# Kernel optimization log

Measured on AMD Instinct MI355X. Metric: run time of the kernel, lower is better.

## Reference

```python
import jax, jax.numpy as jnp
import numpy as np

# Model dims (hardcoded by the hw-accurate numerics: >>6 mean -> d_model=64, 45/256 ~ 1/sqrt(32) -> head_dim=32)
D_MODEL = 64; N_HEADS = 2; HEAD_DIM = 32; D_FF = 256
N_LAYERS = 4; VOCAB = 8192; CTX = 1024; B = 4; T = 1024


def _ste(x, y):
    # forward value y, straight-through gradient of x
    return x + jax.lax.stop_gradient(y - x)


def ste_round_clamp(x, lo, hi):
    return _ste(x, jnp.clip(jnp.round(x), lo, hi))


def ste_round_clamp_int8(x):
    return ste_round_clamp(x, -128.0, 127.0)


def ste_shift_right(x, n):
    s = x * (0.5 ** n)
    return _ste(s, jnp.floor(s))


def ste_hw_int8(x):
    # hardware truncation to signed 8 bits (wrap-around, not clamp)
    return _ste(x, jnp.mod(x + 128.0, 256.0) - 128.0)


def bitlinear_hw(x, w):
    # ternary weights via STE (BitNet b1.58 style), int accumulate, >>6 requant, int8 clamp
    scale = jnp.maximum(jnp.mean(jnp.abs(w)), 1e-5)
    w_t = ste_round_clamp(w / scale, -1.0, 1.0)
    acc = jnp.einsum('btc,oc->bto', x, w_t)
    return ste_round_clamp_int8(ste_shift_right(acc, 6))


def rmsnorm_hw(x, weight):
    x_int = ste_round_clamp_int8(x)
    sum_sq = jnp.sum(x_int * x_int, axis=-1, keepdims=True)
    mean_sq = ste_shift_right(sum_sq, 6)                       # /64 == /d_model
    lut_idx = jnp.clip(ste_shift_right(mean_sq, 6), 0.0, 255.0)
    bin_center = jnp.maximum(lut_idx * 64.0 + 32.0, 1.0)
    inv_rms = ste_round_clamp(16384.0 / jnp.sqrt(bin_center), 0.0, 16383.0)
    w_c = weight + jax.lax.stop_gradient(jnp.clip(weight, -2.0, 2.0) - weight)
    gamma_q = ste_round_clamp(w_c * 1024.0, -32768.0, 32767.0)  # Q5.10
    p1 = ste_shift_right(x_int * inv_rms, 8)
    y = ste_shift_right(p1 * gamma_q, 10)
    return ste_round_clamp_int8(y)


def hw_softmax(scores):
    # 4-segment piecewise-linear exp + uint8 normalization (Softmax.scala)
    m = jnp.max(scores, axis=-1, keepdims=True)
    sh = scores - m
    ea = jnp.where(sh >= -3.0, 256.0 + sh * 64.0,
         jnp.where(sh >= -8.0, 64.0 + (sh + 3.0) * 11.0,
         jnp.where(sh >= -24.0, sh + 24.0, 0.0)))
    s = jnp.maximum(jnp.sum(ea, axis=-1, keepdims=True), 1.0)
    return ste_round_clamp(ea / s * 255.0, 0.0, 255.0)


def _forward(tokens, tok_emb, pos_emb, attn_norm_w, q_w, k_w, v_w, o_w,
             ff_norm_w, up_w, down_w, final_norm_w):
    positions = jnp.arange(T)
    tok_q = ste_round_clamp(tok_emb[tokens] * 1024.0, -32768.0, 32767.0)
    pos_q = ste_round_clamp(pos_emb[positions] * 1024.0, -32768.0, 32767.0)
    x = ste_hw_int8(ste_shift_right(tok_q + pos_q[None], 3))   # [B,T,D]
    causal = jnp.triu(jnp.ones((T, T), dtype=bool), k=1)
    for i in range(N_LAYERS):
        # attention block
        h = rmsnorm_hw(x, attn_norm_w[i])
        q = bitlinear_hw(h, q_w[i]).reshape(B, T, N_HEADS, HEAD_DIM).transpose(0, 2, 1, 3)
        k = bitlinear_hw(h, k_w[i]).reshape(B, T, N_HEADS, HEAD_DIM).transpose(0, 2, 1, 3)
        v = bitlinear_hw(h, v_w[i]).reshape(B, T, N_HEADS, HEAD_DIM).transpose(0, 2, 1, 3)
        scores = ste_shift_right(jnp.einsum('bhqd,bhkd->bhqk', q, k) * 45.0, 8)
        scores = jnp.where(causal, -32767.0, scores)
        probs = hw_softmax(scores)                              # uint8-valued
        a = ste_hw_int8(ste_shift_right(jnp.einsum('bhqk,bhkd->bhqd', probs, v), 8))
        a = a.transpose(0, 2, 1, 3).reshape(B, T, D_MODEL)
        a = bitlinear_hw(a, o_w[i])
        x = ste_hw_int8(x + a)
        # FFN block
        h = rmsnorm_hw(x, ff_norm_w[i])
        u = ste_round_clamp_int8(jax.nn.relu(bitlinear_hw(h, up_w[i])))
        x = ste_hw_int8(x + bitlinear_hw(u, down_w[i]))
    x = rmsnorm_hw(x, final_norm_w)
    # hw logits: INT8 activations x Q5.10 tied embedding, dequant + 1/sqrt(d) scale
    emb_q = ste_round_clamp(tok_emb * 1024.0, -32768.0, 32767.0)
    logits = jnp.einsum('btd,vd->btv', x, emb_q) * (D_MODEL ** -0.5 / 1024.0)
    return logits


def setup_inputs() -> dict:
    key = jax.random.key(0)
    ks = jax.random.split(key, 12)
    std = 0.02
    inp = {
        'tokens': jax.random.randint(ks[0], (B, T), 0, VOCAB),
        'tok_emb': jax.random.normal(ks[1], (VOCAB, D_MODEL), jnp.float32),  # default N(0,1)
        'pos_emb': std * jax.random.normal(ks[2], (CTX, D_MODEL), jnp.float32),
        'attn_norm_w': jnp.ones((N_LAYERS, D_MODEL), jnp.float32),
        'q_w': std * jax.random.normal(ks[3], (N_LAYERS, D_MODEL, D_MODEL), jnp.float32),
        'k_w': std * jax.random.normal(ks[4], (N_LAYERS, D_MODEL, D_MODEL), jnp.float32),
        'v_w': std * jax.random.normal(ks[5], (N_LAYERS, D_MODEL, D_MODEL), jnp.float32),
        'o_w': std * jax.random.normal(ks[6], (N_LAYERS, D_MODEL, D_MODEL), jnp.float32),
        'ff_norm_w': jnp.ones((N_LAYERS, D_MODEL), jnp.float32),
        'up_w': std * jax.random.normal(ks[7], (N_LAYERS, D_FF, D_MODEL), jnp.float32),
        'down_w': std * jax.random.normal(ks[8], (N_LAYERS, D_MODEL, D_FF), jnp.float32),
        'final_norm_w': jnp.ones((D_MODEL,), jnp.float32),
    }
    return inp


def reference(tokens, tok_emb, pos_emb, attn_norm_w, q_w, k_w, v_w, o_w,
              ff_norm_w, up_w, down_w, final_norm_w):
    return _forward(tokens, tok_emb, pos_emb, attn_norm_w, q_w, k_w, v_w, o_w,
                    ff_norm_w, up_w, down_w, final_norm_w)
```

## Files before the change

### kernel.cpp

```cpp
#include <hip/hip_runtime.h>
#include <stdint.h>

#define T_CTX 1024
#define DM 64
#define NH 2
#define HD 32
#define DFF 256
#define NVOCAB 8192

typedef int v4i __attribute__((ext_vector_type(4)));

__device__ __forceinline__ int clampi(int v, int lo, int hi){ return v<lo?lo:(v>hi?hi:v); }
__device__ __forceinline__ int wrap8(int v){ return ((v + 128) & 255) - 128; }
__device__ __forceinline__ int sdot4(int a, int b, int c){ return __builtin_amdgcn_sdot4(a, b, c, false); }

__device__ __forceinline__ int wave_reduce_add(int v){
  #pragma unroll
  for (int off = 1; off < 64; off <<= 1) v += __shfl_xor(v, off, 64);
  return v;
}
__device__ __forceinline__ int wave_reduce_max(int v){
  #pragma unroll
  for (int off = 1; off < 64; off <<= 1){ int o = __shfl_xor(v, off, 64); v = o > v ? o : v; }
  return v;
}

__device__ __forceinline__ int rmsnorm_one(int xv, int g){
  int ss  = wave_reduce_add(xv * xv);
  int ms  = ss >> 6;
  int lut = ms >> 6; if (lut > 255) lut = 255;
  int bc  = lut * 64 + 32;
  int inv = (int)__builtin_rint(16384.0 / __builtin_sqrt((double)bc));
  int p1  = (xv * inv) >> 8;
  int y   = (p1 * g) >> 10;
  return clampi(y, -128, 127);
}

__global__ __launch_bounds__(256) void prep_weights(
    const float* __restrict__ qw, const float* __restrict__ kw, const float* __restrict__ vw,
    const float* __restrict__ ow, const float* __restrict__ uw, const float* __restrict__ dw,
    const float* __restrict__ anw, const float* __restrict__ fnw, const float* __restrict__ finw,
    int8_t* __restrict__ wt, int16_t* __restrict__ gq)
{
  int tid = threadIdx.x;
  int bid = blockIdx.x;
  if (bid < 24) {
    int layer = bid / 6, kind = bid % 6;
    const float* src; int n; int off;
    switch (kind) {
      case 0:  src = qw + layer*4096;  n = 4096;  off = 0;     break;
      case 1:  src = kw + layer*4096;  n = 4096;  off = 4096;  break;
      case 2:  src = vw + layer*4096;  n = 4096;  off = 8192;  break;
      case 3:  src = ow + layer*4096;  n = 4096;  off = 12288; break;
      case 4:  src = uw + layer*16384; n = 16384; off = 16384; break;
      default: src = dw + layer*16384; n = 16384; off = 32768; break;
    }
    __shared__ double sred[256];
    double s = 0.0;
    for (int i = tid; i < n; i += 256) s += (double)__builtin_fabsf(src[i]);
    sred[tid] = s; __syncthreads();
    for (int st = 128; st > 0; st >>= 1){ if (tid < st) sred[tid] += sred[tid + st]; __syncthreads(); }
    float fs = (float)(sred[0] / (double)n);
    if (fs < 1e-5f) fs = 1e-5f;
    int8_t* dst = wt + layer*49152 + off;
    for (int i = tid; i < n; i += 256) {
      int t = (int)__builtin_rintf(src[i] / fs);
      dst[i] = (int8_t)clampi(t, -1, 1);
    }
  } else {
    for (int i = tid; i < 576; i += 256) {
      int norm = i >> 6, c = i & 63;
      const float* wsrc = (norm < 4) ? (anw + norm*64) : (norm < 8) ? (fnw + (norm-4)*64) : finw;
      float wv = wsrc[c];
      float wc = wv < -2.0f ? -2.0f : (wv > 2.0f ? 2.0f : wv);
      gq[i] = (int16_t)clampi((int)__builtin_rintf(wc * 1024.0f), -32768, 32767);
    }
  }
}

__global__ __launch_bounds__(256) void prep_emb_kernel(
    const float* __restrict__ tok_emb, int8_t* __restrict__ elo, int8_t* __restrict__ ehi)
{
  int i = blockIdx.x * 256 + threadIdx.x;
  if (i < NVOCAB * DM) {
    int e  = clampi((int)__builtin_rintf(tok_emb[i] * 1024.0f), -32768, 32767);
    int l  = ((e + 128) & 255) - 128;
    int hh = (e - l) >> 8;
    if (hh > 127) hh = 127;
    elo[i] = (int8_t)l; ehi[i] = (int8_t)hh;
  }
}

__global__ __launch_bounds__(256) void token_stage(
    const int* __restrict__ tokens, const float* __restrict__ tok_emb, const float* __restrict__ pos_emb,
    int8_t* __restrict__ x, const int8_t* __restrict__ aArr,
    int8_t* __restrict__ qA, int8_t* __restrict__ kA, int8_t* __restrict__ vT,
    const int8_t* __restrict__ wt, const int16_t* __restrict__ gq, int8_t* __restrict__ xf,
    int do_embed, int post_layer, int pre_layer, int do_final)
{
  __shared__ int8_t sh8[4][DFF];
  int w = threadIdx.x >> 6, lane = threadIdx.x & 63;
  int t = blockIdx.x * 4 + w;
  int8_t* myS = sh8[w];
  int xv;
  if (do_embed) {
    int tok = tokens[t];
    int s = t & (T_CTX - 1);
    int tq = clampi((int)__builtin_rintf(tok_emb[tok*DM + lane] * 1024.0f), -32768, 32767);
    int pq = clampi((int)__builtin_rintf(pos_emb[s*DM + lane] * 1024.0f), -32768, 32767);
    xv = wrap8((tq + pq) >> 3);
  } else {
    xv = (int)x[t*DM + lane];
  }
  if (post_layer >= 0) {
    const int8_t* wtL = wt + post_layer*49152;
    myS[lane] = aArr[t*DM + lane];
    __syncthreads();
    {
      const int* a4 = (const int*)myS;
      const int* wo = (const int*)(wtL + 12288);
      int acc = 0;
      #pragma unroll
      for (int i = 0; i < 16; i++) acc = sdot4(a4[i], wo[lane*16 + i], acc);
      xv = wrap8(xv + clampi(acc >> 6, -128, 127));
    }
    __syncthreads();
    int h2 = rmsnorm_one(xv, (int)gq[(4 + post_layer)*DM + lane]);
    myS[lane] = (int8_t)h2;
    __syncthreads();
    int uv[4];
    {
      const int* h4 = (const int*)myS;
      const int* wu = (const int*)(wtL + 16384);
      #pragma unroll
      for (int jj = 0; jj < 4; jj++) {
        int j = jj*64 + lane;
        int acc = 0;
        #pragma unroll
        for (int i = 0; i < 16; i++) acc = sdot4(h4[i], wu[j*16 + i], acc);
        int u = clampi(acc >> 6, -128, 127);
        uv[jj] = u < 0 ? 0 : u;
      }
    }
    __syncthreads();
    #pragma unroll
    for (int jj = 0; jj < 4; jj++) myS[jj*64 + lane] = (int8_t)uv[jj];
    __syncthreads();
    {
      const int* u4 = (const int*)myS;
      const int* wd = (const int*)(wtL + 32768);
      int acc = 0;
      #pragma unroll
      for (int i = 0; i < 64; i++) acc = sdot4(u4[i], wd[lane*64 + i], acc);
      xv = wrap8(xv + clampi(acc >> 6, -128, 127));
    }
    __syncthreads();
  }
  x[t*DM + lane] = (int8_t)xv;
  if (pre_layer >= 0) {
    int h = rmsnorm_one(xv, (int)gq[pre_layer*DM + lane]);
    myS[lane] = (int8_t)h;
    __syncthreads();
    const int8_t* wtL = wt + pre_layer*49152;
    const int* h4 = (const int*)myS;
    int b = t >> 10, s = t & (T_CTX - 1);
    int hh = lane >> 5, d = lane & 31;
    int bhh = b*NH + hh;
    {
      const int* wm = (const int*)(wtL + 0);
      int acc = 0;
      #pragma unroll
      for (int i = 0; i < 16; i++) acc = sdot4(h4[i], wm[lane*16 + i], acc);
      qA[(bhh*T_CTX + s)*HD + d] = (int8_t)clampi(acc >> 6, -128, 127);
    }
    {
      const int* wm = (const int*)(wtL + 4096);
      int acc = 0;
      #pragma unroll
      for (int i = 0; i < 16; i++) acc = sdot4(h4[i], wm[lane*16 + i], acc);
      kA[(bhh*T_CTX + s)*HD + d] = (int8_t)clampi(acc >> 6, -128, 127);
    }
    {
      const int* wm = (const int*)(wtL + 8192);
      int acc = 0;
      #pragma unroll
      for (int i = 0; i < 16; i++) acc = sdot4(h4[i], wm[lane*16 + i], acc);
      vT[(bhh*HD + d)*T_CTX + s] = (int8_t)clampi(acc >> 6, -128, 127);
    }
  }
  if (do_final) {
    int h = rmsnorm_one(xv, (int)gq[8*DM + lane]);
    xf[t*DM + lane] = (int8_t)h;
  }
}

__global__ __launch_bounds__(256) void attn_kernel(
    const int8_t* __restrict__ qA, const int8_t* __restrict__ kA, const int8_t* __restrict__ vT,
    int8_t* __restrict__ aOut)
{
  __shared__ int vt32[32*257];
  __shared__ int sp32[4][256];
  int w = threadIdx.x >> 6, lane = threadIdx.x & 63;
  int bh = blockIdx.x & 7, qblk = blockIdx.x >> 3;
  int qi = 1023 - 4*qblk - w;
  int b = bh >> 1, h = bh & 1;
  const int8_t* qBase = qA + bh*(T_CTX*HD);
  const int8_t* kBase = kA + bh*(T_CTX*HD);
  const int8_t* vTbh  = vT + bh*(HD*T_CTX);

  #pragma unroll
  for (int r = 0; r < 8; r++) {
    int d = r*4 + w;
    int4 v = *(const int4*)(vTbh + d*T_CTX + lane*16);
    int* dst = vt32 + d*257 + lane*4;
    dst[0] = v.x; dst[1] = v.y; dst[2] = v.z; dst[3] = v.w;
  }

  const int4* qr = (const int4*)(qBase + qi*HD);
  int4 qa = qr[0], qb = qr[1];
  int sc[16];
  int mloc = -(1 << 30);
  #pragma unroll
  for (int j = 0; j < 16; j++) {
    int k = lane + j*64;
    int s;
    if (k <= qi) {
      const int4* kr = (const int4*)(kBase + k*HD);
      int4 ka = kr[0], kb = kr[1];
      int d = 0;
      d = sdot4(qa.x, ka.x, d); d = sdot4(qa.y, ka.y, d);
      d = sdot4(qa.z, ka.z, d); d = sdot4(qa.w, ka.w, d);
      d = sdot4(qb.x, kb.x, d); d = sdot4(qb.y, kb.y, d);
      d = sdot4(qb.z, kb.z, d); d = sdot4(qb.w, kb.w, d);
      s = (d * 45) >> 8;
    } else s = -(1 << 30);
    sc[j] = s; if (s > mloc) mloc = s;
  }
  int m = wave_reduce_max(mloc);
  int ssum = 0;
  #pragma unroll
  for (int j = 0; j < 16; j++) {
    int k = lane + j*64;
    int e = 0;
    if (k <= qi) {
      int sh = sc[j] - m;
      e = (sh >= -3) ? (256 + sh*64)
        : (sh >= -8) ? (64 + (sh + 3)*11)
        : (sh >= -24) ? (sh + 24) : 0;
    }
    sc[j] = e; ssum += e;
  }
  int s0 = wave_reduce_add(ssum); if (s0 < 1) s0 = 1;
  float sf = (float)s0;
  uint8_t* spb = (uint8_t*)sp32[w];
  #pragma unroll
  for (int j = 0; j < 16; j++) {
    int k = lane + j*64;
    int p = (int)__builtin_rintf((float)sc[j] / sf * 255.0f);
    spb[k] = (uint8_t)clampi(p, 0, 255);
  }
  __syncthreads();

  int dg = lane & 7, kc = lane >> 3;
  const int* vr0 = vt32 + (dg*4 + 0)*257;
  const int* vr1 = vt32 + (dg*4 + 1)*257;
  const int* vr2 = vt32 + (dg*4 + 2)*257;
  const int* vr3 = vt32 + (dg*4 + 3)*257;
  const int* spw = sp32[w];
  int hi0=0, hi1=0, hi2=0, hi3=0, lo0=0, lo1=0, lo2=0, lo3=0;
  int cmax = qi >> 2;
  for (int c = kc; c <= cmax; c += 8) {
    int p4 = spw[c];
    int ph = (p4 >> 1) & 0x7f7f7f7f;
    int pl = p4 & 0x01010101;
    int v0 = vr0[c], v1 = vr1[c], v2 = vr2[c], v3 = vr3[c];
    hi0 = sdot4(ph, v0, hi0); lo0 = sdot4(pl, v0, lo0);
    hi1 = sdot4(ph, v1, hi1); lo1 = sdot4(pl, v1, lo1);
    hi2 = sdot4(ph, v2, hi2); lo2 = sdot4(pl, v2, lo2);
    hi3 = sdot4(ph, v3, hi3); lo3 = sdot4(pl, v3, lo3);
  }
  int a0 = 2*hi0 + lo0, a1 = 2*hi1 + lo1, a2 = 2*hi2 + lo2, a3 = 2*hi3 + lo3;
  #pragma unroll
  for (int off = 8; off < 64; off <<= 1) {
    a0 += __shfl_xor(a0, off, 64);
    a1 += __shfl_xor(a1, off, 64);
    a2 += __shfl_xor(a2, off, 64);
    a3 += __shfl_xor(a3, off, 64);
  }
  if (kc == 0) {
    int r0 = wrap8(a0 >> 8) & 255;
    int r1 = wrap8(a1 >> 8) & 255;
    int r2 = wrap8(a2 >> 8) & 255;
    int r3 = wrap8(a3 >> 8) & 255;
    int packed = r0 | (r1 << 8) | (r2 << 16) | (r3 << 24);
    *(int*)(aOut + (b*T_CTX + qi)*DM + h*HD + dg*4) = packed;
  }
}

__global__ __launch_bounds__(256) void logits_kernel(
    const int8_t* __restrict__ xf, const int8_t* __restrict__ elo, const int8_t* __restrict__ ehi,
    float* __restrict__ out)
{
  int w = threadIdx.x >> 6, lane = threadIdx.x & 63;
  int m = lane & 15, quad = lane >> 4;
  int tokBase = blockIdx.y * 64 + w * 16;
  v4i A = *(const v4i*)(xf + (tokBase + m)*DM + quad*16);
  #pragma unroll
  for (int tile = 0; tile < 8; tile++) {
    int vocBase = blockIdx.x * 128 + tile * 16;
    v4i Blo = *(const v4i*)(elo + (vocBase + m)*DM + quad*16);
    v4i Bhi = *(const v4i*)(ehi + (vocBase + m)*DM + quad*16);
    v4i zero = {0, 0, 0, 0};
    v4i dLo = __builtin_amdgcn_mfma_i32_16x16x64_i8(A, Blo, zero, 0, 0, 0);
    v4i dHi = __builtin_amdgcn_mfma_i32_16x16x64_i8(A, Bhi, zero, 0, 0, 0);
    #pragma unroll
    for (int r = 0; r < 4; r++) {
      int val = dLo[r] + (dHi[r] << 8);
      int row = tokBase + quad*4 + r;
      int col = vocBase + m;
      out[row*NVOCAB + col] = (float)val * 1.220703125e-4f;
    }
  }
}

extern "C" void kernel_launch(void* const* d_in, const int* in_sizes, int n_in,
                              void* d_out, int out_size, void* d_ws, size_t ws_size,
                              hipStream_t stream)
{
  const int*   tokens  = (const int*)d_in[0];
  const float* tok_emb = (const float*)d_in[1];
  const float* pos_emb = (const float*)d_in[2];
  const float* attn_nw = (const float*)d_in[3];
  const float* q_w     = (const float*)d_in[4];
  const float* k_w     = (const float*)d_in[5];
  const float* v_w     = (const float*)d_in[6];
  const float* o_w     = (const float*)d_in[7];
  const float* ff_nw   = (const float*)d_in[8];
  const float* up_w    = (const float*)d_in[9];
  const float* dn_w    = (const float*)d_in[10];
  const float* fin_nw  = (const float*)d_in[11];
  float* out = (float*)d_out;
  char* ws = (char*)d_ws;

  int8_t*  x   = (int8_t*)(ws + 0);
  int8_t*  a   = (int8_t*)(ws + 262144);
  int8_t*  qA  = (int8_t*)(ws + 524288);
  int8_t*  kA  = (int8_t*)(ws + 786432);
  int8_t*  vT  = (int8_t*)(ws + 1048576);
  int8_t*  wt  = (int8_t*)(ws + 1310720);
  int8_t*  elo = (int8_t*)(ws + 1507328);
  int8_t*  ehi = (int8_t*)(ws + 2031616);
  int16_t* gq  = (int16_t*)(ws + 2555904);
  int8_t*  xf  = (int8_t*)(ws + 2560000);

  prep_weights<<<25, 256, 0, stream>>>(q_w, k_w, v_w, o_w, up_w, dn_w, attn_nw, ff_nw, fin_nw, wt, gq);
  prep_emb_kernel<<<2048, 256, 0, stream>>>(tok_emb, elo, ehi);
  token_stage<<<1024, 256, 0, stream>>>(tokens, tok_emb, pos_emb, x, a, qA, kA, vT, wt, gq, xf,
                                        1, -1, 0, 0);
  for (int L = 0; L < 4; L++) {
    attn_kernel<<<2048, 256, 0, stream>>>(qA, kA, vT, a);
    int pre = (L < 3) ? (L + 1) : -1;
    int fin = (L == 3) ? 1 : 0;
    token_stage<<<1024, 256, 0, stream>>>(tokens, tok_emb, pos_emb, x, a, qA, kA, vT, wt, gq, xf,
                                          0, L, pre, fin);
  }
  logits_kernel<<<dim3(64, 64), 256, 0, stream>>>(xf, elo, ehi, out);
}
```

Baseline: 359.8 us.

## Fuse all stages into one persistent cooperative kernel with grid syncs

Replaces the eleven separate kernel launches (weight prep, embedding prep, token stages, attention, logits) with a single cooperative persistent kernel that loops over virtual blocks and uses grid.sync between phases. Attention work is paired (vb and 2047-vb) so causal-length imbalance is evened out per block. This removes launch overhead and inter-kernel gaps, at the cost of grid-wide barriers, a fixed occupancy-limited grid, and shared-memory aliasing across phases.

Result: slower. 923.0 us (+156.5%).

```diff
diff --git a/kernel.cpp b/kernel.cpp
--- a/kernel.cpp
+++ b/kernel.cpp
@@ -1,5 +1,8 @@
 #include <hip/hip_runtime.h>
+#include <hip/hip_cooperative_groups.h>
 #include <stdint.h>
+
+namespace cg = cooperative_groups;
 
 #define T_CTX 1024
 #define DM 64
@@ -36,72 +39,18 @@
   return clampi(y, -128, 127);
 }
 
-__global__ __launch_bounds__(256) void prep_weights(
-    const float* __restrict__ qw, const float* __restrict__ kw, const float* __restrict__ vw,
-    const float* __restrict__ ow, const float* __restrict__ uw, const float* __restrict__ dw,
-    const float* __restrict__ anw, const float* __restrict__ fnw, const float* __restrict__ finw,
-    int8_t* __restrict__ wt, int16_t* __restrict__ gq)
-{
-  int tid = threadIdx.x;
-  int bid = blockIdx.x;
-  if (bid < 24) {
-    int layer = bid / 6, kind = bid % 6;
-    const float* src; int n; int off;
-    switch (kind) {
-      case 0:  src = qw + layer*4096;  n = 4096;  off = 0;     break;
-      case 1:  src = kw + layer*4096;  n = 4096;  off = 4096;  break;
-      case 2:  src = vw + layer*4096;  n = 4096;  off = 8192;  break;
-      case 3:  src = ow + layer*4096;  n = 4096;  off = 12288; break;
-      case 4:  src = uw + layer*16384; n = 16384; off = 16384; break;
-      default: src = dw + layer*16384; n = 16384; off = 32768; break;
-    }
-    __shared__ double sred[256];
-    double s = 0.0;
-    for (int i = tid; i < n; i += 256) s += (double)__builtin_fabsf(src[i]);
-    sred[tid] = s; __syncthreads();
-    for (int st = 128; st > 0; st >>= 1){ if (tid < st) sred[tid] += sred[tid + st]; __syncthreads(); }
-    float fs = (float)(sred[0] / (double)n);
-    if (fs < 1e-5f) fs = 1e-5f;
-    int8_t* dst = wt + layer*49152 + off;
-    for (int i = tid; i < n; i += 256) {
-      int t = (int)__builtin_rintf(src[i] / fs);
-      dst[i] = (int8_t)clampi(t, -1, 1);
-    }
-  } else {
-    for (int i = tid; i < 576; i += 256) {
-      int norm = i >> 6, c = i & 63;
-      const float* wsrc = (norm < 4) ? (anw + norm*64) : (norm < 8) ? (fnw + (norm-4)*64) : finw;
-      float wv = wsrc[c];
-      float wc = wv < -2.0f ? -2.0f : (wv > 2.0f ? 2.0f : wv);
-      gq[i] = (int16_t)clampi((int)__builtin_rintf(wc * 1024.0f), -32768, 32767);
-    }
-  }
-}
-
-__global__ __launch_bounds__(256) void prep_emb_kernel(
-    const float* __restrict__ tok_emb, int8_t* __restrict__ elo, int8_t* __restrict__ ehi)
-{
-  int i = blockIdx.x * 256 + threadIdx.x;
-  if (i < NVOCAB * DM) {
-    int e  = clampi((int)__builtin_rintf(tok_emb[i] * 1024.0f), -32768, 32767);
-    int l  = ((e + 128) & 255) - 128;
-    int hh = (e - l) >> 8;
-    if (hh > 127) hh = 127;
-    elo[i] = (int8_t)l; ehi[i] = (int8_t)hh;
-  }
-}
-
-__global__ __launch_bounds__(256) void token_stage(
-    const int* __restrict__ tokens, const float* __restrict__ tok_emb, const float* __restrict__ pos_emb,
-    int8_t* __restrict__ x, const int8_t* __restrict__ aArr,
+__device__ __forceinline__ void token_phase(
+    int blk, const int* __restrict__ tokens, const float* __restrict__ tok_emb,
+    const float* __restrict__ pos_emb, int8_t* __restrict__ x, const int8_t* __restrict__ aArr,
     int8_t* __restrict__ qA, int8_t* __restrict__ kA, int8_t* __restrict__ vT,
     const int8_t* __restrict__ wt, const int16_t* __restrict__ gq, int8_t* __restrict__ xf,
-    int do_embed, int post_layer, int pre_layer, int do_final)
+    int do_embed, int post_layer, int pre_layer, int do_final,
+    int8_t (*sh8)[DFF])
 {
-  __shared__ int8_t sh8[4][DFF];
   int w = threadIdx.x >> 6, lane = threadIdx.x & 63;
-  int t = blockIdx.x * 4 + w;
+  int t = blk * 4 + w;
   int8_t* myS = sh8[w];
+  __syncthreads();
   int xv;
   if (do_embed) {
     int tok = tokens[t];
@@ -194,19 +143,20 @@
   }
 }
 
-__global__ __launch_bounds__(256) void attn_kernel(
-    const int8_t* __restrict__ qA, const int8_t* __restrict__ kA, const int8_t* __restrict__ vT,
-    int8_t* __restrict__ aOut)
+__device__ __forceinline__ void attn_phase(
+    int vb, const int8_t* __restrict__ qA, const int8_t* __restrict__ kA,
+    const int8_t* __restrict__ vT, int8_t* __restrict__ aOut,
+    int* vt32, int (*sp32)[256])
 {
-  __shared__ int vt32[32*257];
-  __shared__ int sp32[4][256];
   int w = threadIdx.x >> 6, lane = threadIdx.x & 63;
-  int bh = blockIdx.x & 7, qblk = blockIdx.x >> 3;
+  int bh = vb & 7, qblk = vb >> 3;
   int qi = 1023 - 4*qblk - w;
   int b = bh >> 1, h = bh & 1;
   const int8_t* qBase = qA + bh*(T_CTX*HD);
   const int8_t* kBase = kA + bh*(T_CTX*HD);
   const int8_t* vTbh  = vT + bh*(HD*T_CTX);
+
+  __syncthreads();
 
   #pragma unroll
   for (int r = 0; r < 8; r++) {
@@ -297,28 +247,114 @@
   }
 }
 
-__global__ __launch_bounds__(256) void logits_kernel(
-    const int8_t* __restrict__ xf, const int8_t* __restrict__ elo, const int8_t* __restrict__ ehi,
-    float* __restrict__ out)
+__global__ __launch_bounds__(256, 4) void fused(
+    const int* __restrict__ tokens, const float* __restrict__ tok_emb, const float* __restrict__ pos_emb,
+    const float* __restrict__ anw, const float* __restrict__ qw, const float* __restrict__ kw,
+    const float* __restrict__ vw, const float* __restrict__ ow, const float* __restrict__ fnw,
+    const float* __restrict__ uw, const float* __restrict__ dw, const float* __restrict__ finw,
+    float* __restrict__ out, char* __restrict__ ws)
 {
-  int w = threadIdx.x >> 6, lane = threadIdx.x & 63;
-  int m = lane & 15, quad = lane >> 4;
-  int tokBase = blockIdx.y * 64 + w * 16;
-  v4i A = *(const v4i*)(xf + (tokBase + m)*DM + quad*16);
-  #pragma unroll
-  for (int tile = 0; tile < 8; tile++) {
-    int vocBase = blockIdx.x * 128 + tile * 16;
-    v4i Blo = *(const v4i*)(elo + (vocBase + m)*DM + quad*16);
-    v4i Bhi = *(const v4i*)(ehi + (vocBase + m)*DM + quad*16);
-    v4i zero = {0, 0, 0, 0};
-    v4i dLo = __builtin_amdgcn_mfma_i32_16x16x64_i8(A, Blo, zero, 0, 0, 0);
-    v4i dHi = __builtin_amdgcn_mfma_i32_16x16x64_i8(A, Bhi, zero, 0, 0, 0);
+  __shared__ __align__(16) int smem[32*257 + 4*256];
+  int* vt32 = smem;
+  int (*sp32)[256] = (int(*)[256])(smem + 32*257);
+  int8_t (*sh8)[DFF] = (int8_t(*)[DFF])smem;
+  double* sred = (double*)smem;
+
+  int8_t*  x   = (int8_t*)(ws + 0);
+  int8_t*  a   = (int8_t*)(ws + 262144);
+  int8_t*  qA  = (int8_t*)(ws + 524288);
+  int8_t*  kA  = (int8_t*)(ws + 786432);
+  int8_t*  vT  = (int8_t*)(ws + 1048576);
+  int8_t*  wt  = (int8_t*)(ws + 1310720);
+  int8_t*  elo = (int8_t*)(ws + 1507328);
+  int8_t*  ehi = (int8_t*)(ws + 2031616);
+  int16_t* gq  = (int16_t*)(ws + 2555904);
+  int8_t*  xf  = (int8_t*)(ws + 2560000);
+
+  cg::grid_group grid = cg::this_grid();
+  int tid = threadIdx.x, bid = blockIdx.x, nb = gridDim.x;
+
+  if (bid < 24) {
+    int layer = bid / 6, kind = bid % 6;
+    const float* src; int n; int off;
+    switch (kind) {
+      case 0:  src = qw + layer*4096;  n = 4096;  off = 0;     break;
+      case 1:  src = kw + layer*4096;  n = 4096;  off = 4096;  break;
+      case 2:  src = vw + layer*4096;  n = 4096;  off = 8192;  break;
+      case 3:  src = ow + layer*4096;  n = 4096;  off = 12288; break;
+      case 4:  src = uw + layer*16384; n = 16384; off = 16384; break;
+      default: src = dw + layer*16384; n = 16384; off = 32768; break;
+    }
+    double s = 0.0;
+    for (int i = tid; i < n; i += 256) s += (double)__builtin_fabsf(src[i]);
+    sred[tid] = s; __syncthreads();
+    for (int st = 128; st > 0; st >>= 1){ if (tid < st) sred[tid] += sred[tid + st]; __syncthreads(); }
+    float fs = (float)(sred[0] / (double)n);
+    if (fs < 1e-5f) fs = 1e-5f;
+    int8_t* dst = wt + layer*49152 + off;
+    for (int i = tid; i < n; i += 256) {
+      int t = (int)__builtin_rintf(src[i] / fs);
+      dst[i] = (int8_t)clampi(t, -1, 1);
+    }
+  } else if (bid == 24) {
+    for (int i = tid; i < 576; i += 256) {
+      int norm = i >> 6, c = i & 63;
+      const float* wsrc = (norm < 4) ? (anw + norm*64) : (norm < 8) ? (fnw + (norm-4)*64) : finw;
+      float wv = wsrc[c];
+      float wc = wv < -2.0f ? -2.0f : (wv > 2.0f ? 2.0f : wv);
+      gq[i] = (int16_t)clampi((int)__builtin_rintf(wc * 1024.0f), -32768, 32767);
+    }
+  } else {
+    int base = (bid - 25)*256 + tid;
+    int stride = (nb - 25)*256;
+    for (int i = base; i < NVOCAB*DM; i += stride) {
+      int e  = clampi((int)__builtin_rintf(tok_emb[i] * 1024.0f), -32768, 32767);
+      int l  = ((e + 128) & 255) - 128;
+      int hh = (e - l) >> 8;
+      if (hh > 127) hh = 127;
+      elo[i] = (int8_t)l; ehi[i] = (int8_t)hh;
+    }
+  }
+  grid.sync();
+
+  for (int vb = bid; vb < 1024; vb += nb)
+    token_phase(vb, tokens, tok_emb, pos_emb, x, a, qA, kA, vT, wt, gq, xf, 1, -1, 0, 0, sh8);
+  grid.sync();
+
+  for (int L = 0; L < 4; L++) {
+    for (int vb = bid; vb < 1024; vb += nb) {
+      attn_phase(vb,        qA, kA, vT, a, vt32, sp32);
+      attn_phase(2047 - vb, qA, kA, vT, a, vt32, sp32);
+    }
+    grid.sync();
+    int pre = (L < 3) ? (L + 1) : -1;
+    int fin = (L == 3) ? 1 : 0;
+    for (int vb = bid; vb < 1024; vb += nb)
+      token_phase(vb, tokens, tok_emb, pos_emb, x, a, qA, kA, vT, wt, gq, xf, 0, L, pre, fin, sh8);
+    grid.sync();
+  }
+
+  for (int vb = bid; vb < 4096; vb += nb) {
+    int by = vb >> 6, bx = vb & 63;
+    int w = tid >> 6, lane = tid & 63;
+    int m = lane & 15, quad = lane >> 4;
+    int tokBase = by * 64 + w * 16;
+    v4i A = *(const v4i*)(xf + (tokBase + m)*DM + quad*16);
     #pragma unroll
-    for (int r = 0; r < 4; r++) {
-      int val = dLo[r] + (dHi[r] << 8);
-      int row = tokBase + quad*4 + r;
-      int col = vocBase + m;
-      out[row*NVOCAB + col] = (float)val * 1.220703125e-4f;
+    for (int tile = 0; tile < 8; tile++) {
+      int vocBase = bx * 128 + tile * 16;
+      v4i Blo = *(const v4i*)(elo + (vocBase + m)*DM + quad*16);
+      v4i Bhi = *(const v4i*)(ehi + (vocBase + m)*DM + quad*16);
+      v4i zero = {0, 0, 0, 0};
+      v4i dLo = __builtin_amdgcn_mfma_i32_16x16x64_i8(A, Blo, zero, 0, 0, 0);
+      v4i dHi = __builtin_amdgcn_mfma_i32_16x16x64_i8(A, Bhi, zero, 0, 0, 0);
+      #pragma unroll
+      for (int r = 0; r < 4; r++) {
+        int val = dLo[r] + (dHi[r] << 8);
+        int row = tokBase + quad*4 + r;
+        int col = vocBase + m;
+        out[row*NVOCAB + col] = (float)val * 1.220703125e-4f;
+      }
     }
   }
 }
@@ -342,27 +378,22 @@
   float* out = (float*)d_out;
   char* ws = (char*)d_ws;
 
-  int8_t*  x   = (int8_t*)(ws + 0);
-  int8_t*  a   = (int8_t*)(ws + 262144);
-  int8_t*  qA  = (int8_t*)(ws + 524288);
-  int8_t*  kA  = (int8_t*)(ws + 786432);
-  int8_t*  vT  = (int8_t*)(ws + 1048576);
-  int8_t*  wt  = (int8_t*)(ws + 1310720);
-  int8_t*  elo = (int8_t*)(ws + 1507328);
-  int8_t*  ehi = (int8_t*)(ws + 2031616);
-  int16_t* gq  = (int16_t*)(ws + 2555904);
-  int8_t*  xf  = (int8_t*)(ws + 2560000);
-
-  prep_weights<<<25, 256, 0, stream>>>(q_w, k_w, v_w, o_w, up_w, dn_w, attn_nw, ff_nw, fin_nw, wt, gq);
-  prep_emb_kernel<<<2048, 256, 0, stream>>>(tok_emb, elo, ehi);
-  token_stage<<<1024, 256, 0, stream>>>(tokens, tok_emb, pos_emb, x, a, qA, kA, vT, wt, gq, xf,
-                                        1, -1, 0, 0);
-  for (int L = 0; L < 4; L++) {
-    attn_kernel<<<2048, 256, 0, stream>>>(qA, kA, vT, a);
-    int pre = (L < 3) ? (L + 1) : -1;
-    int fin = (L == 3) ? 1 : 0;
-    token_stage<<<1024, 256, 0, stream>>>(tokens, tok_emb, pos_emb, x, a, qA, kA, vT, wt, gq, xf,
-                                          0, L, pre, fin);
-  }
-  logits_kernel<<<dim3(64, 64), 256, 0, stream>>>(xf, elo, ehi, out);
-}
+  static int nblk = 0;
+  if (nblk == 0) {
+    int perCU = 0;
+    if (hipOccupancyMaxActiveBlocksPerMultiprocessor(&perCU, (const void*)fused, 256, 0) != hipSuccess
+        || perCU < 1) perCU = 4;
+    int dev = 0; hipGetDevice(&dev);
+    hipDeviceProp_t prop{};
+    int ncu = 256;
+    if (hipGetDeviceProperties(&prop, dev) == hipSuccess && prop.multiProcessorCount > 0)
+      ncu = prop.multiProcessorCount;
+    long tot = (long)perCU * (long)ncu;
+    nblk = (int)(tot < 1024 ? tot : 1024);
+    if (nblk < 26) nblk = 26;
+  }
+
+  void* args[] = { &tokens, &tok_emb, &pos_emb, &attn_nw, &q_w, &k_w, &v_w, &o_w,
+                   &ff_nw, &up_w, &dn_w, &fin_nw, &out, &ws };
+  hipLaunchCooperativeKernel((const void*)fused, dim3(nblk), dim3(256), args, 0, stream);
+}
```

## Fuse attention with per-token MLP stage and merge prep kernels

Applied to the files above, without the earlier changes.

Attention for two queries times two heads per block is now fused with the output projection, FFN, next-layer norm and QKV projection, so the attention output never goes through global memory. Q/K/V are double-buffered across layers so the fused kernel can write the next layer's inputs while other blocks still read the current ones. The two prep kernels become one launch, and V is read straight from global memory instead of being staged in shared memory. In exchange, half the waves sit idle during the MLP phase, the 2048-block grid means each block handles fewer tokens, and the uncached V reads may cost bandwidth.

New measurement: 429.7 us. 19.4% more time.

```diff
diff --git a/kernel.cpp b/kernel.cpp
--- a/kernel.cpp
+++ b/kernel.cpp
@@ -36,11 +36,13 @@
   return clampi(y, -128, 127);
 }
 
-__global__ __launch_bounds__(256) void prep_weights(
+__global__ __launch_bounds__(256) void prep_all(
     const float* __restrict__ qw, const float* __restrict__ kw, const float* __restrict__ vw,
     const float* __restrict__ ow, const float* __restrict__ uw, const float* __restrict__ dw,
     const float* __restrict__ anw, const float* __restrict__ fnw, const float* __restrict__ finw,
-    int8_t* __restrict__ wt, int16_t* __restrict__ gq)
+    const float* __restrict__ tok_emb,
+    int8_t* __restrict__ wt, int16_t* __restrict__ gq,
+    int8_t* __restrict__ elo, int8_t* __restrict__ ehi)
 {
   int tid = threadIdx.x;
   int bid = blockIdx.x;
@@ -67,7 +69,7 @@
       int t = (int)__builtin_rintf(src[i] / fs);
       dst[i] = (int8_t)clampi(t, -1, 1);
     }
-  } else {
+  } else if (bid == 24) {
     for (int i = tid; i < 576; i += 256) {
       int norm = i >> 6, c = i & 63;
       const float* wsrc = (norm < 4) ? (anw + norm*64) : (norm < 8) ? (fnw + (norm-4)*64) : finw;
@@ -75,146 +77,84 @@
       float wc = wv < -2.0f ? -2.0f : (wv > 2.0f ? 2.0f : wv);
       gq[i] = (int16_t)clampi((int)__builtin_rintf(wc * 1024.0f), -32768, 32767);
     }
-  }
-}
-
-__global__ __launch_bounds__(256) void prep_emb_kernel(
-    const float* __restrict__ tok_emb, int8_t* __restrict__ elo, int8_t* __restrict__ ehi)
-{
-  int i = blockIdx.x * 256 + threadIdx.x;
-  if (i < NVOCAB * DM) {
-    int e  = clampi((int)__builtin_rintf(tok_emb[i] * 1024.0f), -32768, 32767);
-    int l  = ((e + 128) & 255) - 128;
-    int hh = (e - l) >> 8;
-    if (hh > 127) hh = 127;
-    elo[i] = (int8_t)l; ehi[i] = (int8_t)hh;
-  }
-}
-
-__global__ __launch_bounds__(256) void token_stage(
+  } else {
+    int i = (bid - 25)*256 + tid;
+    if (i < NVOCAB * DM) {
+      int e  = clampi((int)__builtin_rintf(tok_emb[i] * 1024.0f), -32768, 32767);
+      int l  = ((e + 128) & 255) - 128;
+      int hh = (e - l) >> 8;
+      if (hh > 127) hh = 127;
+      elo[i] = (int8_t)l; ehi[i] = (int8_t)hh;
+    }
+  }
+}
+
+__global__ __launch_bounds__(256) void embed_pre0(
     const int* __restrict__ tokens, const float* __restrict__ tok_emb, const float* __restrict__ pos_emb,
-    int8_t* __restrict__ x, const int8_t* __restrict__ aArr,
-    int8_t* __restrict__ qA, int8_t* __restrict__ kA, int8_t* __restrict__ vT,
-    const int8_t* __restrict__ wt, const int16_t* __restrict__ gq, int8_t* __restrict__ xf,
-    int do_embed, int post_layer, int pre_layer, int do_final)
-{
-  __shared__ int8_t sh8[4][DFF];
+    int8_t* __restrict__ x, int8_t* __restrict__ qA, int8_t* __restrict__ kA, int8_t* __restrict__ vT,
+    const int8_t* __restrict__ wt, const int16_t* __restrict__ gq)
+{
+  __shared__ int8_t sh8[4][64];
   int w = threadIdx.x >> 6, lane = threadIdx.x & 63;
   int t = blockIdx.x * 4 + w;
-  int8_t* myS = sh8[w];
-  int xv;
-  if (do_embed) {
-    int tok = tokens[t];
-    int s = t & (T_CTX - 1);
-    int tq = clampi((int)__builtin_rintf(tok_emb[tok*DM + lane] * 1024.0f), -32768, 32767);
-    int pq = clampi((int)__builtin_rintf(pos_emb[s*DM + lane] * 1024.0f), -32768, 32767);
-    xv = wrap8((tq + pq) >> 3);
-  } else {
-    xv = (int)x[t*DM + lane];
-  }
-  if (post_layer >= 0) {
-    const int8_t* wtL = wt + post_layer*49152;
-    myS[lane] = aArr[t*DM + lane];
-    __syncthreads();
-    {
-      const int* a4 = (const int*)myS;
-      const int* wo = (const int*)(wtL + 12288);
-      int acc = 0;
-      #pragma unroll
-      for (int i = 0; i < 16; i++) acc = sdot4(a4[i], wo[lane*16 + i], acc);
-      xv = wrap8(xv + clampi(acc >> 6, -128, 127));
-    }
-    __syncthreads();
-    int h2 = rmsnorm_one(xv, (int)gq[(4 + post_layer)*DM + lane]);
-    myS[lane] = (int8_t)h2;
-    __syncthreads();
-    int uv[4];
-    {
-      const int* h4 = (const int*)myS;
-      const int* wu = (const int*)(wtL + 16384);
-      #pragma unroll
-      for (int jj = 0; jj < 4; jj++) {
-        int j = jj*64 + lane;
-        int acc = 0;
-        #pragma unroll
-        for (int i = 0; i < 16; i++) acc = sdot4(h4[i], wu[j*16 + i], acc);
-        int u = clampi(acc >> 6, -128, 127);
-        uv[jj] = u < 0 ? 0 : u;
-      }
-    }
-    __syncthreads();
-    #pragma unroll
-    for (int jj = 0; jj < 4; jj++) myS[jj*64 + lane] = (int8_t)uv[jj];
-    __syncthreads();
-    {
-      const int* u4 = (const int*)myS;
-      const int* wd = (const int*)(wtL + 32768);
-      int acc = 0;
-      #pragma unroll
-      for (int i = 0; i < 64; i++) acc = sdot4(u4[i], wd[lane*64 + i], acc);
-      xv = wrap8(xv + clampi(acc >> 6, -128, 127));
-    }
-    __syncthreads();
-  }
+  int tok = tokens[t];
+  int s = t & (T_CTX - 1);
+  int tq = clampi((int)__builtin_rintf(tok_emb[tok*DM + lane] * 1024.0f), -32768, 32767);
+  int pq = clampi((int)__builtin_rintf(pos_emb[s*DM + lane] * 1024.0f), -32768, 32767);
+  int xv = wrap8((tq + pq) >> 3);
   x[t*DM + lane] = (int8_t)xv;
-  if (pre_layer >= 0) {
-    int h = rmsnorm_one(xv, (int)gq[pre_layer*DM + lane]);
-    myS[lane] = (int8_t)h;
-    __syncthreads();
-    const int8_t* wtL = wt + pre_layer*49152;
-    const int* h4 = (const int*)myS;
-    int b = t >> 10, s = t & (T_CTX - 1);
-    int hh = lane >> 5, d = lane & 31;
-    int bhh = b*NH + hh;
-    {
-      const int* wm = (const int*)(wtL + 0);
-      int acc = 0;
-      #pragma unroll
-      for (int i = 0; i < 16; i++) acc = sdot4(h4[i], wm[lane*16 + i], acc);
-      qA[(bhh*T_CTX + s)*HD + d] = (int8_t)clampi(acc >> 6, -128, 127);
-    }
-    {
-      const int* wm = (const int*)(wtL + 4096);
-      int acc = 0;
-      #pragma unroll
-      for (int i = 0; i < 16; i++) acc = sdot4(h4[i], wm[lane*16 + i], acc);
-      kA[(bhh*T_CTX + s)*HD + d] = (int8_t)clampi(acc >> 6, -128, 127);
-    }
-    {
-      const int* wm = (const int*)(wtL + 8192);
-      int acc = 0;
-      #pragma unroll
-      for (int i = 0; i < 16; i++) acc = sdot4(h4[i], wm[lane*16 + i], acc);
-      vT[(bhh*HD + d)*T_CTX + s] = (int8_t)clampi(acc >> 6, -128, 127);
-    }
-  }
-  if (do_final) {
-    int h = rmsnorm_one(xv, (int)gq[8*DM + lane]);
-    xf[t*DM + lane] = (int8_t)h;
-  }
-}
-
-__global__ __launch_bounds__(256) void attn_kernel(
+  int h = rmsnorm_one(xv, (int)gq[lane]);
+  sh8[w][lane] = (int8_t)h;
+  __syncthreads();
+  const int* h4 = (const int*)sh8[w];
+  int b = t >> 10;
+  int hh = lane >> 5, d = lane & 31;
+  int bhh = b*NH + hh;
+  const int8_t* wtL = wt;
+  {
+    const int* wm = (const int*)(wtL + 0);
+    int acc = 0;
+    #pragma unroll
+    for (int i = 0; i < 16; i++) acc = sdot4(h4[i], wm[lane*16 + i], acc);
+    qA[(bhh*T_CTX + s)*HD + d] = (int8_t)clampi(acc >> 6, -128, 127);
+  }
+  {
+    const int* wm = (const int*)(wtL + 4096);
+    int acc = 0;
+    #pragma unroll
+    for (int i = 0; i < 16; i++) acc = sdot4(h4[i], wm[lane*16 + i], acc);
+    kA[(bhh*T_CTX + s)*HD + d] = (int8_t)clampi(acc >> 6, -128, 127);
+  }
+  {
+    const int* wm = (const int*)(wtL + 8192);
+    int acc = 0;
+    #pragma unroll
+    for (int i = 0; i < 16; i++) acc = sdot4(h4[i], wm[lane*16 + i], acc);
+    vT[(bhh*HD + d)*T_CTX + s] = (int8_t)clampi(acc >> 6, -128, 127);
+  }
+}
+
+__global__ __launch_bounds__(256) void layer_kernel(
     const int8_t* __restrict__ qA, const int8_t* __restrict__ kA, const int8_t* __restrict__ vT,
-    int8_t* __restrict__ aOut)
-{
-  __shared__ int vt32[32*257];
+    int8_t* __restrict__ x, int8_t* __restrict__ qN, int8_t* __restrict__ kN, int8_t* __restrict__ vN,
+    const int8_t* __restrict__ wt, const int16_t* __restrict__ gq, int8_t* __restrict__ xf,
+    int L, int pre_layer, int do_final)
+{
   __shared__ int sp32[4][256];
+  __shared__ int sh_a32[2][16];
+  __shared__ int8_t sh8[2][256];
+
   int w = threadIdx.x >> 6, lane = threadIdx.x & 63;
-  int bh = blockIdx.x & 7, qblk = blockIdx.x >> 3;
-  int qi = 1023 - 4*qblk - w;
-  int b = bh >> 1, h = bh & 1;
+  int blk = blockIdx.x;
+  int b = blk & 3;
+  int s0 = 1022 - 2*(blk >> 2);
+  int tl = w >> 1;
+  int qi = s0 + tl;
+  int h = w & 1;
+  int bh = b*NH + h;
   const int8_t* qBase = qA + bh*(T_CTX*HD);
   const int8_t* kBase = kA + bh*(T_CTX*HD);
   const int8_t* vTbh  = vT + bh*(HD*T_CTX);
-
-  #pragma unroll
-  for (int r = 0; r < 8; r++) {
-    int d = r*4 + w;
-    int4 v = *(const int4*)(vTbh + d*T_CTX + lane*16);
-    int* dst = vt32 + d*257 + lane*4;
-    dst[0] = v.x; dst[1] = v.y; dst[2] = v.z; dst[3] = v.w;
-  }
 
   const int4* qr = (const int4*)(qBase + qi*HD);
   int4 qa = qr[0], qb = qr[1];
@@ -250,8 +190,8 @@
     }
     sc[j] = e; ssum += e;
   }
-  int s0 = wave_reduce_add(ssum); if (s0 < 1) s0 = 1;
-  float sf = (float)s0;
+  int s0sum = wave_reduce_add(ssum); if (s0sum < 1) s0sum = 1;
+  float sf = (float)s0sum;
   uint8_t* spb = (uint8_t*)sp32[w];
   #pragma unroll
   for (int j = 0; j < 16; j++) {
@@ -262,10 +202,10 @@
   __syncthreads();
 
   int dg = lane & 7, kc = lane >> 3;
-  const int* vr0 = vt32 + (dg*4 + 0)*257;
-  const int* vr1 = vt32 + (dg*4 + 1)*257;
-  const int* vr2 = vt32 + (dg*4 + 2)*257;
-  const int* vr3 = vt32 + (dg*4 + 3)*257;
+  const int* vr0 = (const int*)(vTbh + (dg*4 + 0)*T_CTX);
+  const int* vr1 = (const int*)(vTbh + (dg*4 + 1)*T_CTX);
+  const int* vr2 = (const int*)(vTbh + (dg*4 + 2)*T_CTX);
+  const int* vr3 = (const int*)(vTbh + (dg*4 + 3)*T_CTX);
   const int* spw = sp32[w];
   int hi0=0, hi1=0, hi2=0, hi3=0, lo0=0, lo1=0, lo2=0, lo3=0;
   int cmax = qi >> 2;
@@ -293,7 +233,96 @@
     int r2 = wrap8(a2 >> 8) & 255;
     int r3 = wrap8(a3 >> 8) & 255;
     int packed = r0 | (r1 << 8) | (r2 << 16) | (r3 << 24);
-    *(int*)(aOut + (b*T_CTX + qi)*DM + h*HD + dg*4) = packed;
+    sh_a32[tl][h*8 + dg] = packed;
+  }
+  __syncthreads();
+
+  int t = b*T_CTX + s0 + w;
+  int xv = 0;
+  const int8_t* wtL = wt + L*49152;
+  if (w < 2) {
+    xv = (int)x[t*DM + lane];
+    {
+      const int* a4 = sh_a32[w];
+      const int* wo = (const int*)(wtL + 12288);
+      int acc = 0;
+      #pragma unroll
+      for (int i = 0; i < 16; i++) acc = sdot4(a4[i], wo[lane*16 + i], acc);
+      xv = wrap8(xv + clampi(acc >> 6, -128, 127));
+    }
+    int h2 = rmsnorm_one(xv, (int)gq[(4 + L)*DM + lane]);
+    sh8[w][lane] = (int8_t)h2;
+  }
+  __syncthreads();
+  if (w < 2) {
+    int8_t* myS = sh8[w];
+    const int* h4 = (const int*)myS;
+    int uv[4];
+    {
+      const int* wu = (const int*)(wtL + 16384);
+      #pragma unroll
+      for (int jj = 0; jj < 4; jj++) {
+        int j = jj*64 + lane;
+        int acc = 0;
+        #pragma unroll
+        for (int i = 0; i < 16; i++) acc = sdot4(h4[i], wu[j*16 + i], acc);
+        int u = clampi(acc >> 6, -128, 127);
+        uv[jj] = u < 0 ? 0 : u;
+      }
+    }
+    #pragma unroll
+    for (int jj = 0; jj < 4; jj++) myS[jj*64 + lane] = (int8_t)uv[jj];
+  }
+  __syncthreads();
+  if (w < 2) {
+    const int* u4 = (const int*)sh8[w];
+    {
+      const int* wd = (const int*)(wtL + 32768);
+      int acc = 0;
+      #pragma unroll
+      for (int i = 0; i < 64; i++) acc = sdot4(u4[i], wd[lane*64 + i], acc);
+      xv = wrap8(xv + clampi(acc >> 6, -128, 127));
+    }
+    x[t*DM + lane] = (int8_t)xv;
+  }
+  if (pre_layer >= 0) {
+    if (w < 2) {
+      int hp = rmsnorm_one(xv, (int)gq[pre_layer*DM + lane]);
+      sh8[w][lane] = (int8_t)hp;
+    }
+    __syncthreads();
+    if (w < 2) {
+      const int* h4 = (const int*)sh8[w];
+      const int8_t* wtP = wt + pre_layer*49152;
+      int s = s0 + w;
+      int hh = lane >> 5, d = lane & 31;
+      int bhh = b*NH + hh;
+      {
+        const int* wm = (const int*)(wtP + 0);
+        int acc = 0;
+        #pragma unroll
+        for (int i = 0; i < 16; i++) acc = sdot4(h4[i], wm[lane*16 + i], acc);
+        qN[(bhh*T_CTX + s)*HD + d] = (int8_t)clampi(acc >> 6, -128, 127);
+      }
+      {
+        const int* wm = (const int*)(wtP + 4096);
+        int acc = 0;
+        #pragma unroll
+        for (int i = 0; i < 16; i++) acc = sdot4(h4[i], wm[lane*16 + i], acc);
+        kN[(bhh*T_CTX + s)*HD + d] = (int8_t)clampi(acc >> 6, -128, 127);
+      }
+      {
+        const int* wm = (const int*)(wtP + 8192);
+        int acc = 0;
+        #pragma unroll
+        for (int i = 0; i < 16; i++) acc = sdot4(h4[i], wm[lane*16 + i], acc);
+        vN[(bhh*HD + d)*T_CTX + s] = (int8_t)clampi(acc >> 6, -128, 127);
+      }
+    }
+  }
+  if (do_final && w < 2) {
+    int hf = rmsnorm_one(xv, (int)gq[8*DM + lane]);
+    xf[t*DM + lane] = (int8_t)hf;
   }
 }
 
@@ -342,27 +371,29 @@
   float* out = (float*)d_out;
   char* ws = (char*)d_ws;
 
-  int8_t*  x   = (int8_t*)(ws + 0);
-  int8_t*  a   = (int8_t*)(ws + 262144);
-  int8_t*  qA  = (int8_t*)(ws + 524288);
-  int8_t*  kA  = (int8_t*)(ws + 786432);
-  int8_t*  vT  = (int8_t*)(ws + 1048576);
-  int8_t*  wt  = (int8_t*)(ws + 1310720);
-  int8_t*  elo = (int8_t*)(ws + 1507328);
-  int8_t*  ehi = (int8_t*)(ws + 2031616);
-  int16_t* gq  = (int16_t*)(ws + 2555904);
-  int8_t*  xf  = (int8_t*)(ws + 2560000);
-
-  prep_weights<<<25, 256, 0, stream>>>(q_w, k_w, v_w, o_w, up_w, dn_w, attn_nw, ff_nw, fin_nw, wt, gq);
-  prep_emb_kernel<<<2048, 256, 0, stream>>>(tok_emb, elo, ehi);
-  token_stage<<<1024, 256, 0, stream>>>(tokens, tok_emb, pos_emb, x, a, qA, kA, vT, wt, gq, xf,
-                                        1, -1, 0, 0);
+  int8_t*  x    = (int8_t*)(ws + 0);
+  int8_t*  qA0  = (int8_t*)(ws + 262144);
+  int8_t*  kA0  = (int8_t*)(ws + 524288);
+  int8_t*  vT0  = (int8_t*)(ws + 786432);
+  int8_t*  qA1  = (int8_t*)(ws + 1048576);
+  int8_t*  kA1  = (int8_t*)(ws + 1310720);
+  int8_t*  vT1  = (int8_t*)(ws + 1572864);
+  int8_t*  wt   = (int8_t*)(ws + 1835008);
+  int8_t*  elo  = (int8_t*)(ws + 2031616);
+  int8_t*  ehi  = (int8_t*)(ws + 2555904);
+  int16_t* gq   = (int16_t*)(ws + 3080192);
+  int8_t*  xf   = (int8_t*)(ws + 3081344);
+
+  prep_all<<<2073, 256, 0, stream>>>(q_w, k_w, v_w, o_w, up_w, dn_w, attn_nw, ff_nw, fin_nw,
+                                     tok_emb, wt, gq, elo, ehi);
+  embed_pre0<<<1024, 256, 0, stream>>>(tokens, tok_emb, pos_emb, x, qA0, kA0, vT0, wt, gq);
   for (int L = 0; L < 4; L++) {
-    attn_kernel<<<2048, 256, 0, stream>>>(qA, kA, vT, a);
+    int8_t* qC = (L & 1) ? qA1 : qA0;  int8_t* qX = (L & 1) ? qA0 : qA1;
+    int8_t* kC = (L & 1) ? kA1 : kA0;  int8_t* kX = (L & 1) ? kA0 : kA1;
+    int8_t* vC = (L & 1) ? vT1 : vT0;  int8_t* vX = (L & 1) ? vT0 : vT1;
     int pre = (L < 3) ? (L + 1) : -1;
     int fin = (L == 3) ? 1 : 0;
-    token_stage<<<1024, 256, 0, stream>>>(tokens, tok_emb, pos_emb, x, a, qA, kA, vT, wt, gq, xf,
-                                          0, L, pre, fin);
+    layer_kernel<<<2048, 256, 0, stream>>>(qC, kC, vC, x, qX, kX, vX, wt, gq, xf, L, pre, fin);
   }
   logits_kernel<<<dim3(64, 64), 256, 0, stream>>>(xf, elo, ehi, out);
 }
```
